# Optimization experiments

Hardware: AMD Instinct MI355X
Metric: run time of the kernel (lower is better)

The kernel has to match this reference:

```python
import jax, jax.numpy as jnp
import numpy as np

TOP_K = 5
MIN_DIST = 10
SALIENCY_THR = 0.1
BLUR_K = 5
BLUR_SIGMA = 1.0
BORDER = 12
Q = 0.9
CAND_MULT = 16  # candidate pool = TOP_K * CAND_MULT before min-dist suppression


def _hann(n):
    # torch.hann_window(n, periodic=False)
    return 0.5 * (1.0 - jnp.cos(2.0 * jnp.pi * jnp.arange(n, dtype=jnp.float32) / (n - 1)))


def _gauss_kernel2d():
    r = BLUR_K // 2
    x = jnp.arange(-r, r + 1, dtype=jnp.float32)
    g = jnp.exp(-(x ** 2) / (2.0 * BLUR_SIGMA ** 2))
    g = g / g.sum()
    k2 = g[:, None] * g[None, :]
    return k2[None, None]  # [1,1,k,k]


def _phase_saliency(img):
    """Phase-spectrum saliency: window -> FFT -> phase-only -> iFFT -> |.|^2 -> blur -> minmax norm -> border mask."""
    B, C, H, W = img.shape
    win = (_hann(H)[:, None] * _hann(W)[None, :])[None, None]  # [1,1,H,W]
    x = img * win
    f = jnp.fft.fft2(x)
    recon = jnp.fft.ifft2(jnp.exp(1j * jnp.angle(f)))
    sal = jnp.abs(recon) ** 2
    pad = BLUR_K // 2
    sal = jax.lax.conv_general_dilated(
        sal, _gauss_kernel2d(), (1, 1), [(pad, pad), (pad, pad)],
        dimension_numbers=("NCHW", "OIHW", "NCHW"))
    mn = sal.min(axis=(2, 3), keepdims=True)
    mx = sal.max(axis=(2, 3), keepdims=True)
    sal = (sal - mn) / (mx - mn + 1e-8)
    border = jnp.zeros((H, W), jnp.float32).at[BORDER:H - BORDER, BORDER:W - BORDER].set(1.0)
    return sal * border


def _dynamic_threshold(sal):
    # thr = value of the k-th largest pixel, k = (1-q)*N  (matches torch.topk(flat,k)[..., -1])
    B = sal.shape[0]
    flat = sal.reshape(B, -1)
    n = flat.shape[1]
    k = max(1, int((1.0 - Q) * n))
    vals = jax.lax.top_k(flat, k)[0]
    return vals[:, -1]  # [B]


def _select_points(sal2d, thr):
    """Greedy min-dist (NMS-style) selection of up to TOP_K peaks above thr. Returns (coords[K,2] xy, labels[K])."""
    H, W = sal2d.shape
    M = TOP_K * CAND_MULT
    scores = jnp.where(sal2d >= thr, sal2d, -jnp.inf).reshape(-1)
    vals, idx = jax.lax.top_k(scores, M)
    ys = (idx // W).astype(jnp.float32)
    xs = (idx % W).astype(jnp.float32)
    pts = jnp.stack([xs, ys], axis=-1)  # (x, y) ordering as in original
    valid = jnp.isfinite(vals)

    def body(i, state):
        keep, cnt = state
        d2 = jnp.sum((pts - pts[i]) ** 2, axis=-1)
        near_kept = jnp.any((d2 < float(MIN_DIST ** 2)) & keep)
        ok = valid[i] & (~near_kept) & (cnt < TOP_K)
        return keep.at[i].set(ok), cnt + ok.astype(jnp.int32)

    keep, _ = jax.lax.fori_loop(0, M, body, (jnp.zeros((M,), bool), jnp.int32(0)))
    order = jnp.argsort(jnp.where(keep, 0, 1).astype(jnp.int32))  # stable: kept (in score order) first
    sel = order[:TOP_K]
    kept = keep[sel]
    coords = jnp.where(kept[:, None], pts[sel], -1.0)
    labels = jnp.where(kept, 1, -1).astype(jnp.int32)
    return coords, labels


def setup_inputs() -> dict:
    key = jax.random.key(0)
    img = jax.random.uniform(key, (16, 1, 512, 512), dtype=jnp.float32)
    return {"img": img}


def reference(img):
    sal = _phase_saliency(img)                      # [B,1,H,W]
    thr = jnp.maximum(_dynamic_threshold(sal), SALIENCY_THR)  # dynamic_thr_mode='max'
    coords, labels = jax.vmap(_select_points)(sal[:, 0], thr)
    return coords, labels, sal
```

## Files before the change

### kernel.cpp

```cpp
#include <hip/hip_runtime.h>
#include <math.h>

#define BATCH 16
#define HW 262144
#define KSEL 26214
#define MCAND 80
#define TOPK 5
#define CAP 2048
#define ZEROWORDS 204816


#define GW0 0.05448868454964294f
#define GW1 0.24420134200323332f
#define GW2 0.40261994689424746f

#define FILL_TW512(nthr)                                       \
    for (int i_ = threadIdx.x; i_ < 256; i_ += (nthr)) {       \
        float rev_ = -(float)i_ * (1.0f / 512.0f);             \
        float s_ = __builtin_amdgcn_sinf(rev_);                \
        float c_ = __builtin_amdgcn_cosf(rev_);                \
        tws[i_] = s_;        twc[i_] = c_;                     \
        tws[i_ + 256] = -s_; twc[i_ + 256] = -c_;              \
    }

#define RP(a) ((a) + ((a) >> 4))
#define RSZ 544

#define R4_FWD(rr, ri, q, s4)                                                 \
    {                                                                          \
        const int log2n = 9 - 2 * (s4);                                        \
        const int log2m = log2n - 2;                                           \
        const int m = 1 << log2m;                                              \
        int r = (q) & (m - 1);                                                 \
        int j0 = (((q) >> log2m) << log2n) + r;                                \
        float a0x = rr[RP(j0)],       a0y = ri[RP(j0)];                        \
        float a1x = rr[RP(j0 + m)],   a1y = ri[RP(j0 + m)];                    \
        float a2x = rr[RP(j0 + 2*m)], a2y = ri[RP(j0 + 2*m)];                  \
        float a3x = rr[RP(j0 + 3*m)], a3y = ri[RP(j0 + 3*m)];                  \
        float s02x = a0x + a2x, s02y = a0y + a2y;                              \
        float d02x = a0x - a2x, d02y = a0y - a2y;                              \
        float s13x = a1x + a3x, s13y = a1y + a3y;                              \
        float d13x = a1x - a3x, d13y = a1y - a3y;                              \
        float y0x = s02x + s13x, y0y = s02y + s13y;                            \
        float y2x = s02x - s13x, y2y = s02y - s13y;                            \
        float y1x = d02x + d13y, y1y = d02y - d13x;                            \
        float y3x = d02x - d13y, y3y = d02y + d13x;                            \
        int e = r << (2 * (s4));                                               \
        float c1 = twc[e],   s1 = tws[e];                                      \
        float c2 = twc[2*e], s2 = tws[2*e];                                    \
        float c3 = twc[3*e], s3 = tws[3*e];                                    \
        rr[RP(j0)]       = y0x;             ri[RP(j0)]       = y0y;            \
        rr[RP(j0 + m)]   = y1x*c1 - y1y*s1; ri[RP(j0 + m)]   = y1x*s1 + y1y*c1;\
        rr[RP(j0 + 2*m)] = y2x*c2 - y2y*s2; ri[RP(j0 + 2*m)] = y2x*s2 + y2y*c2;\
        rr[RP(j0 + 3*m)] = y3x*c3 - y3y*s3; ri[RP(j0 + 3*m)] = y3x*s3 + y3y*c3;\
    }

#define R4_INV(rr, ri, q, s4)                                                 \
    {                                                                          \
        const int log2n = 9 - 2 * (s4);                                        \
        const int log2m = log2n - 2;                                           \
        const int m = 1 << log2m;                                              \
        int r = (q) & (m - 1);                                                 \
        int j0 = (((q) >> log2m) << log2n) + r;                                \
        float a0x = rr[RP(j0)],       a0y = ri[RP(j0)];                        \
        float a1x = rr[RP(j0 + m)],   a1y = ri[RP(j0 + m)];                    \
        float a2x = rr[RP(j0 + 2*m)], a2y = ri[RP(j0 + 2*m)];                  \
        float a3x = rr[RP(j0 + 3*m)], a3y = ri[RP(j0 + 3*m)];                  \
        int e = r << (2 * (s4));                                               \
        float c1 = twc[e],   s1 = tws[e];                                      \
        float c2 = twc[2*e], s2 = tws[2*e];                                    \
        float c3 = twc[3*e], s3 = tws[3*e];                                    \
        float t1x = a1x*c1 + a1y*s1,  t1y = a1y*c1 - a1x*s1;                   \
        float t2x = a2x*c2 + a2y*s2,  t2y = a2y*c2 - a2x*s2;                   \
        float t3x = a3x*c3 + a3y*s3,  t3y = a3y*c3 - a3x*s3;                   \
        float s02x = a0x + t2x, s02y = a0y + t2y;                              \
        float d02x = a0x - t2x, d02y = a0y - t2y;                              \
        float s13x = t1x + t3x, s13y = t1y + t3y;                              \
        float d13x = t1x - t3x, d13y = t1y - t3y;                              \
        rr[RP(j0)]       = s02x + s13x;  ri[RP(j0)]       = s02y + s13y;       \
        rr[RP(j0 + 2*m)] = s02x - s13x;  ri[RP(j0 + 2*m)] = s02y - s13y;       \
        rr[RP(j0 + m)]   = d02x - d13y;  ri[RP(j0 + m)]   = d02y + d13x;       \
        rr[RP(j0 + 3*m)] = d02x + d13y;  ri[RP(j0 + 3*m)] = d02y - d13x;       \
    }

__global__ void k_win_rowfft(const float* __restrict__ img, float2* __restrict__ A) {
    __shared__ float re[2 * RSZ], im[2 * RSZ];
    __shared__ float twc[512], tws[512];
    int t = threadIdx.x;
    FILL_TW512(256)
    int lr = t >> 7;
    int u  = t & 127;
    int row = blockIdx.x * 2 + lr;
    int h = row & 511;
    float wr = 0.5f * (1.0f - __builtin_amdgcn_cosf((float)h * (1.0f / 511.0f)));
    const float* p = img + (size_t)row * 512;
    float* rr = re + lr * RSZ;
    float* ri = im + lr * RSZ;
    {
        int i0 = u * 4;
        float4 v = *reinterpret_cast<const float4*>(p + i0);
        float w0 = 0.5f * (1.0f - __builtin_amdgcn_cosf((float)(i0 + 0) * (1.0f / 511.0f)));
        float w1 = 0.5f * (1.0f - __builtin_amdgcn_cosf((float)(i0 + 1) * (1.0f / 511.0f)));
        float w2 = 0.5f * (1.0f - __builtin_amdgcn_cosf((float)(i0 + 2) * (1.0f / 511.0f)));
        float w3 = 0.5f * (1.0f - __builtin_amdgcn_cosf((float)(i0 + 3) * (1.0f / 511.0f)));
        rr[RP(i0 + 0)] = v.x * wr * w0;  ri[RP(i0 + 0)] = 0.0f;
        rr[RP(i0 + 1)] = v.y * wr * w1;  ri[RP(i0 + 1)] = 0.0f;
        rr[RP(i0 + 2)] = v.z * wr * w2;  ri[RP(i0 + 2)] = 0.0f;
        rr[RP(i0 + 3)] = v.w * wr * w3;  ri[RP(i0 + 3)] = 0.0f;
    }
    __syncthreads();
    R4_FWD(rr, ri, u, 0)  __syncthreads();
    R4_FWD(rr, ri, u, 1)  __syncthreads();
    R4_FWD(rr, ri, u, 2)  __syncthreads();
    R4_FWD(rr, ri, u, 3)  __syncthreads();
    #pragma unroll
    for (int kk = 0; kk < 2; ++kk) {
        int j = (kk * 128 + u) << 1;
        float ax = rr[RP(j)], ay = ri[RP(j)], bx = rr[RP(j + 1)], by = ri[RP(j + 1)];
        rr[RP(j)]     = ax + bx;  ri[RP(j)]     = ay + by;
        rr[RP(j + 1)] = ax - bx;  ri[RP(j + 1)] = ay - by;
    }
    __syncthreads();
    float2* out = A + (size_t)row * 512;
    #pragma unroll
    for (int k2 = 0; k2 < 2; ++k2) {
        int i = u * 4 + k2 * 2;
        float4 v = make_float4(rr[RP(i)], ri[RP(i)], rr[RP(i + 1)], ri[RP(i + 1)]);
        *reinterpret_cast<float4*>(&out[i]) = v;
    }
}

#define CSTR 514
__global__ __launch_bounds__(512) void k_colfft(float2* __restrict__ X) {
    __shared__ float re[16 * CSTR];
    __shared__ float im[16 * CSTR];
    __shared__ float twc[512], tws[512];
    int b = blockIdx.x >> 5;
    int c0 = (blockIdx.x & 31) * 16;
    int t = threadIdx.x;
    FILL_TW512(512)
    float2* base = X + (size_t)b * HW + c0;
    #pragma unroll
    for (int ii = 0; ii < 8; ++ii) {
        int linear = ii * 512 + t;
        int cp = linear & 7;
        int e  = linear >> 3;
        const float4 v = *reinterpret_cast<const float4*>(&base[(size_t)e * 512 + cp * 2]);
        int a0 = (cp * 2) * CSTR + e;
        int a1 = a0 + CSTR;
        re[a0] = v.x; im[a0] = v.y;
        re[a1] = v.z; im[a1] = v.w;
    }
    __syncthreads();
    int c = t & 15, tt = t >> 4;
    float* cr = re + c * CSTR;
    float* ci = im + c * CSTR;

    for (int s4 = 0; s4 < 4; ++s4) {
        int log2n = 9 - 2 * s4;
        int log2m = log2n - 2;
        int m = 1 << log2m;
        #pragma unroll
        for (int kk = 0; kk < 4; ++kk) {
            int q = kk * 32 + tt;
            int r = q & (m - 1);
            int j0 = ((q >> log2m) << log2n) + r;
            float a0x = cr[j0],       a0y = ci[j0];
            float a1x = cr[j0 + m],   a1y = ci[j0 + m];
            float a2x = cr[j0 + 2*m], a2y = ci[j0 + 2*m];
            float a3x = cr[j0 + 3*m], a3y = ci[j0 + 3*m];
            float s02x = a0x + a2x, s02y = a0y + a2y;
            float d02x = a0x - a2x, d02y = a0y - a2y;
            float s13x = a1x + a3x, s13y = a1y + a3y;
            float d13x = a1x - a3x, d13y = a1y - a3y;
            float y0x = s02x + s13x, y0y = s02y + s13y;
            float y2x = s02x - s13x, y2y = s02y - s13y;
            float y1x = d02x + d13y, y1y = d02y - d13x;
            float y3x = d02x - d13y, y3y = d02y + d13x;
            int e = r << (2 * s4);
            float c1 = twc[e],   s1 = tws[e];
            float c2 = twc[2*e], s2 = tws[2*e];
            float c3 = twc[3*e], s3 = tws[3*e];
            cr[j0]       = y0x;                 ci[j0]       = y0y;
            cr[j0 + m]   = y1x*c1 - y1y*s1;     ci[j0 + m]   = y1x*s1 + y1y*c1;
            cr[j0 + 2*m] = y2x*c2 - y2y*s2;     ci[j0 + 2*m] = y2x*s2 + y2y*c2;
            cr[j0 + 3*m] = y3x*c3 - y3y*s3;     ci[j0 + 3*m] = y3x*s3 + y3y*c3;
        }
        __syncthreads();
    }
    #pragma unroll
    for (int kk = 0; kk < 8; ++kk) {
        int j = (kk * 32 + tt) << 1;
        float ax = cr[j], ay = ci[j], bx = cr[j+1], by = ci[j+1];
        cr[j]   = ax + bx; ci[j]   = ay + by;
        cr[j+1] = ax - bx; ci[j+1] = ay - by;
    }
    __syncthreads();
    #pragma unroll
    for (int ii = 0; ii < 16; ++ii) {
        int linear = ii * 512 + t;
        int cc = linear & 15, e = linear >> 4;
        int a = cc * CSTR + e;
        float x = re[a], y = im[a];
        float m2 = x * x + y * y;
        if (m2 > 0.0f) {
            float inv = rsqrtf(m2);
            re[a] = x * inv; im[a] = y * inv;
        } else {
            re[a] = 1.0f; im[a] = 0.0f;
        }
    }
    __syncthreads();
    #pragma unroll
    for (int kk = 0; kk < 8; ++kk) {
        int j = (kk * 32 + tt) << 1;
        float ax = cr[j], ay = ci[j], bx = cr[j+1], by = ci[j+1];
        cr[j]   = ax + bx; ci[j]   = ay + by;
        cr[j+1] = ax - bx; ci[j+1] = ay - by;
    }
    __syncthreads();
    for (int s4 = 3; s4 >= 0; --s4) {
        int log2n = 9 - 2 * s4;
        int log2m = log2n - 2;
        int m = 1 << log2m;
        #pragma unroll
        for (int kk = 0; kk < 4; ++kk) {
            int q = kk * 32 + tt;
            int r = q & (m - 1);
            int j0 = ((q >> log2m) << log2n) + r;
            float a0x = cr[j0],       a0y = ci[j0];
            float a1x = cr[j0 + m],   a1y = ci[j0 + m];
            float a2x = cr[j0 + 2*m], a2y = ci[j0 + 2*m];
            float a3x = cr[j0 + 3*m], a3y = ci[j0 + 3*m];
            int e = r << (2 * s4);
            float c1 = twc[e],   s1 = tws[e];
            float c2 = twc[2*e], s2 = tws[2*e];
            float c3 = twc[3*e], s3 = tws[3*e];
            float t1x = a1x*c1 + a1y*s1,  t1y = a1y*c1 - a1x*s1;
            float t2x = a2x*c2 + a2y*s2,  t2y = a2y*c2 - a2x*s2;
            float t3x = a3x*c3 + a3y*s3,  t3y = a3y*c3 - a3x*s3;
            float s02x = a0x + t2x, s02y = a0y + t2y;
            float d02x = a0x - t2x, d02y = a0y - t2y;
            float s13x = t1x + t3x, s13y = t1y + t3y;
            float d13x = t1x - t3x, d13y = t1y - t3y;
            cr[j0]       = s02x + s13x;   ci[j0]       = s02y + s13y;
            cr[j0 + 2*m] = s02x - s13x;   ci[j0 + 2*m] = s02y - s13y;
            cr[j0 + m]   = d02x - d13y;   ci[j0 + m]   = d02y + d13x;
            cr[j0 + 3*m] = d02x + d13y;   ci[j0 + 3*m] = d02y - d13x;
        }
        __syncthreads();
    }
    #pragma unroll
    for (int ii = 0; ii < 8; ++ii) {
        int linear = ii * 512 + t;
        int cp = linear & 7;
        int e  = linear >> 3;
        int a0 = (cp * 2) * CSTR + e;
        int a1 = a0 + CSTR;
        float4 v = make_float4(re[a0], im[a0], re[a1], im[a1]);
        *reinterpret_cast<float4*>(&base[(size_t)e * 512 + cp * 2]) = v;
    }
}

__global__ void k_mag_hblur(const float2* __restrict__ X, float* __restrict__ out) {
    __shared__ float re[2 * RSZ], im[2 * RSZ];
    __shared__ float twc[512], tws[512];
    int t = threadIdx.x;
    FILL_TW512(256)
    int lr = t >> 7;
    int u  = t & 127;
    int row = blockIdx.x * 2 + lr;
    const float2* p = X + (size_t)row * 512;
    float* rr = re + lr * RSZ;
    float* ri = im + lr * RSZ;
    #pragma unroll
    for (int k2 = 0; k2 < 2; ++k2) {
        int i = u * 4 + k2 * 2;
        float4 v = *reinterpret_cast<const float4*>(&p[i]);
        rr[RP(i)]     = v.x; ri[RP(i)]     = v.y;
        rr[RP(i + 1)] = v.z; ri[RP(i + 1)] = v.w;
    }
    __syncthreads();
    #pragma unroll
    for (int kk = 0; kk < 2; ++kk) {
        int j = (kk * 128 + u) << 1;
        float ax = rr[RP(j)], ay = ri[RP(j)], bx = rr[RP(j + 1)], by = ri[RP(j + 1)];
        rr[RP(j)]     = ax + bx;  ri[RP(j)]     = ay + by;
        rr[RP(j + 1)] = ax - bx;  ri[RP(j + 1)] = ay - by;
    }
    __syncthreads();
    R4_INV(rr, ri, u, 3)  __syncthreads();
    R4_INV(rr, ri, u, 2)  __syncthreads();
    R4_INV(rr, ri, u, 1)  __syncthreads();
    R4_INV(rr, ri, u, 0)  __syncthreads();
    const float s = 3.814697265625e-06f;
    #pragma unroll
    for (int k4 = 0; k4 < 4; ++k4) {
        int i = u * 4 + k4;
        float x = rr[RP(i)] * s, y = ri[RP(i)] * s;
        ri[RP(i)] = x * x + y * y;
    }
    __syncthreads();
    float* o = out + (size_t)row * 512;
    float4 res;
    #pragma unroll
    for (int k4 = 0; k4 < 4; ++k4) {
        int i = u * 4 + k4;
        float acc = GW2 * ri[RP(i)];
        if (i >= 1)   acc += GW1 * ri[RP(i - 1)];
        if (i >= 2)   acc += GW0 * ri[RP(i - 2)];
        if (i <= 510) acc += GW1 * ri[RP(i + 1)];
        if (i <= 509) acc += GW0 * ri[RP(i + 2)];
        ((float*)&res)[k4] = acc;
    }
    *reinterpret_cast<float4*>(o + u * 4) = res;
}

__global__ void k_vblur(const float* __restrict__ in, float* __restrict__ out,
                        float* __restrict__ pmn, float* __restrict__ pmx,
                        unsigned int* __restrict__ zr) {
    __shared__ float smn[256];
    __shared__ float smx[256];
    int t = threadIdx.x;
    int gi = blockIdx.x * 256 + t;
    if (gi < ZEROWORDS) zr[gi] = 0u;
    int i = gi * 4;
    int y = (i >> 9) & 511;
    const float4 c = *reinterpret_cast<const float4*>(in + i);
    float4 acc = make_float4(GW2 * c.x, GW2 * c.y, GW2 * c.z, GW2 * c.w);
    if (y >= 1) {
        const float4 v = *reinterpret_cast<const float4*>(in + i - 512);
        acc.x += GW1 * v.x; acc.y += GW1 * v.y; acc.z += GW1 * v.z; acc.w += GW1 * v.w;
    }
    if (y >= 2) {
        const float4 v = *reinterpret_cast<const float4*>(in + i - 1024);
        acc.x += GW0 * v.x; acc.y += GW0 * v.y; acc.z += GW0 * v.z; acc.w += GW0 * v.w;
    }
    if (y <= 510) {
        const float4 v = *reinterpret_cast<const float4*>(in + i + 512);
        acc.x += GW1 * v.x; acc.y += GW1 * v.y; acc.z += GW1 * v.z; acc.w += GW1 * v.w;
    }
    if (y <= 509) {
        const float4 v = *reinterpret_cast<const float4*>(in + i + 1024);
        acc.x += GW0 * v.x; acc.y += GW0 * v.y; acc.z += GW0 * v.z; acc.w += GW0 * v.w;
    }
    *reinterpret_cast<float4*>(out + i) = acc;
    float lmn = fminf(fminf(acc.x, acc.y), fminf(acc.z, acc.w));
    float lmx = fmaxf(fmaxf(acc.x, acc.y), fmaxf(acc.z, acc.w));
    smn[t] = lmn; smx[t] = lmx;
    __syncthreads();
    for (int s = 128; s > 0; s >>= 1) {
        if (t < s) { smn[t] = fminf(smn[t], smn[t + s]); smx[t] = fmaxf(smx[t], smx[t + s]); }
        __syncthreads();
    }
    if (t == 0) { pmn[blockIdx.x] = smn[0]; pmx[blockIdx.x] = smx[0]; }
}

__global__ void k_norm_hist(const float* __restrict__ in, const float* __restrict__ pmn,
                            const float* __restrict__ pmx, float* __restrict__ out,
                            unsigned int* __restrict__ g) {
    __shared__ unsigned int h[4096];
    __shared__ float smn[256], smx[256];
    int t = threadIdx.x;
    int b = blockIdx.x >> 5;
    int base = b * HW + (blockIdx.x & 31) * 8192;
    smn[t] = pmn[b * 256 + t];
    smx[t] = pmx[b * 256 + t];
    for (int i = t; i < 4096; i += 256) h[i] = 0u;
    __syncthreads();
    for (int s = 128; s > 0; s >>= 1) {
        if (t < s) { smn[t] = fminf(smn[t], smn[t + s]); smx[t] = fmaxf(smx[t], smx[t + s]); }
        __syncthreads();
    }
    float mn = smn[0], mx = smx[0];
    float inv = 1.0f / (mx - mn + 1e-8f);
    for (int j = 0; j < 32; ++j) {
        int idx = base + j * 256 + t;
        float v = (in[idx] - mn) * inv;
        int xx = idx & 511, yy = (idx >> 9) & 511;
        bool inside = (xx >= 12) && (xx < 500) && (yy >= 12) && (yy < 500);
        v = inside ? v : 0.0f;
        out[idx] = v;
        atomicAdd(&h[__float_as_uint(v) >> 20], 1u);
    }
    __syncthreads();
    unsigned int* gb = g + b * 4096;
    for (int i = t; i < 4096; i += 256)
        if (h[i]) atomicAdd(&gb[i], h[i]);
}

__device__ void radix_step(const unsigned int* __restrict__ h, int nbins, int krem,
                           int t, unsigned int* tsuf, int* sbin, int* skrem) {
    int bpt = nbins >> 8;
    unsigned int s = 0;
    for (int j = 0; j < bpt; ++j) s += h[t * bpt + j];
    tsuf[t] = s;
    __syncthreads();
    #pragma unroll
    for (int off = 1; off < 256; off <<= 1) {
        unsigned int v = (t + off < 256) ? tsuf[t + off] : 0u;
        __syncthreads();
        tsuf[t] += v;
        __syncthreads();
    }
    if ((int)tsuf[t] >= krem && (t == 255 || (int)tsuf[t + 1] < krem))
        *sbin = t;
    __syncthreads();
    int seg = *sbin;
    int krem2 = krem - (seg < 255 ? (int)tsuf[seg + 1] : 0);
    __syncthreads();
    if (t < bpt) {
        unsigned int L = 0;
        for (int j = t; j < bpt; ++j) L += h[seg * bpt + j];
        unsigned int hv = h[seg * bpt + t];
        if ((int)L >= krem2 && (int)(L - hv) < krem2) {
            *sbin  = seg * bpt + t;
            *skrem = krem2 - (int)(L - hv);
        }
    }
    __syncthreads();
}

__global__ void k_hist2(const float* __restrict__ sal, const unsigned int* __restrict__ g1,
                        unsigned int* __restrict__ gA, unsigned int* __restrict__ gB,
                        unsigned int* prefA1, int* kremA1, unsigned int* prefB1, int* kremB1) {
    __shared__ unsigned int hA[4096];
    __shared__ unsigned int hB[4096];
    __shared__ unsigned int tsuf[256];
    __shared__ int sbin, skrem;
    int t = threadIdx.x;
    int b = blockIdx.x >> 5;
    int start = (blockIdx.x & 31) * 8192;
    for (int i = t; i < 4096; i += 256) { hA[i] = 0u; hB[i] = 0u; }
    radix_step(g1 + b * 4096, 4096, KSEL, t, tsuf, &sbin, &skrem);
    unsigned int pA = (unsigned int)sbin; int krA = skrem;
    radix_step(g1 + b * 4096, 4096, MCAND, t, tsuf, &sbin, &skrem);
    unsigned int pB = (unsigned int)sbin; int krB = skrem;
    if (t == 0 && (blockIdx.x & 31) == 0) {
        prefA1[b] = pA; kremA1[b] = krA; prefB1[b] = pB; kremB1[b] = krB;
    }
    const float* p = sal + (size_t)b * HW;
    for (int j = 0; j < 32; ++j) {
        unsigned int u = __float_as_uint(p[start + j * 256 + t]);
        unsigned int hi = u >> 20, mid = (u >> 8) & 4095u;
        if (hi == pA) atomicAdd(&hA[mid], 1u);
        if (hi == pB) atomicAdd(&hB[mid], 1u);
    }
    __syncthreads();
    unsigned int* ga = gA + b * 4096;
    unsigned int* gb2 = gB + b * 4096;
    for (int i = t; i < 4096; i += 256) {
        if (hA[i]) atomicAdd(&ga[i], hA[i]);
        if (hB[i]) atomicAdd(&gb2[i], hB[i]);
    }
}

__global__ void k_hist3collect(const float* __restrict__ sal,
                               const unsigned int* __restrict__ gA2, const unsigned int* __restrict__ gB2,
                               const unsigned int* prefA1, const int* kremA1,
                               const unsigned int* prefB1, const int* kremB1,
                               unsigned int* __restrict__ gA3,
                               unsigned int* prefA24, int* kremA2,
                               float* __restrict__ candv, int* __restrict__ candi,
                               int* __restrict__ ccnt) {
    __shared__ unsigned int hA[256];
    __shared__ unsigned int tsuf[256];
    __shared__ int sbin, skrem;
    int t = threadIdx.x;
    int b = blockIdx.x >> 5;
    int start = (blockIdx.x & 31) * 8192;
    hA[t] = 0u;
    radix_step(gA2 + b * 4096, 4096, kremA1[b], t, tsuf, &sbin, &skrem);
    unsigned int pA = (prefA1[b] << 12) | (unsigned int)sbin;
    int krA2 = skrem;
    radix_step(gB2 + b * 4096, 4096, kremB1[b], t, tsuf, &sbin, &skrem);
    unsigned int cutB = ((prefB1[b] << 12) | (unsigned int)sbin) << 8;
    if (t == 0 && (blockIdx.x & 31) == 0) { prefA24[b] = pA; kremA2[b] = krA2; }
    const float* p = sal + (size_t)b * HW;
    for (int j = 0; j < 32; ++j) {
        int i = start + j * 256 + t;
        unsigned int u = __float_as_uint(p[i]);
        if ((u >> 8) == pA) atomicAdd(&hA[u & 255u], 1u);
        if (u >= cutB) {
            int pos = atomicAdd(&ccnt[b], 1);
            if (pos < CAP) { candv[b * CAP + pos] = p[i]; candi[b * CAP + pos] = i; }
        }
    }
    __syncthreads();
    if (hA[t]) atomicAdd(&gA3[b * 256 + t], hA[t]);
}

__global__ void k_final(const unsigned int* __restrict__ gA3,
                        const unsigned int* prefA24, const int* kremA2,
                        const float* __restrict__ candv, const int* __restrict__ candi,
                        const int* __restrict__ ccnt, float* __restrict__ out) {
    __shared__ float cval[CAP];
    __shared__ int   cidx[CAP];
    __shared__ int   si[MCAND];
    __shared__ float svv[MCAND];
    __shared__ float sx[MCAND];
    __shared__ float sy[MCAND];
    __shared__ unsigned long long nearLo[MCAND];
    __shared__ unsigned long long nearHi[MCAND];
    __shared__ unsigned int tsuf[256];
    __shared__ int sbin, skrem;
    int b = blockIdx.x, t = threadIdx.x;
    radix_step(gA3 + b * 256, 256, kremA2[b], t, tsuf, &sbin, &skrem);
    float thr = fmaxf(__uint_as_float((prefA24[b] << 8) | (unsigned int)sbin), 0.1f);
    int n = min(ccnt[b], CAP);
    for (int i = t; i < n; i += 256) { cval[i] = candv[b * CAP + i]; cidx[i] = candi[b * CAP + i]; }
    __syncthreads();
    int m = min(n, MCAND);
    for (int i = t; i < n; i += 256) {
        float vi = cval[i]; int ii = cidx[i];
        int rank = 0;
        for (int j = 0; j < n; j++) {
            float vj = cval[j];
            if (vj > vi || (vj == vi && cidx[j] < ii)) rank++;
        }
        if (rank < MCAND) { si[rank] = ii; svv[rank] = vi; }
    }
    __syncthreads();
    for (int i = t; i < m; i += 256) {
        sx[i] = (float)(si[i] & 511);
        sy[i] = (float)(si[i] >> 9);
    }
    __syncthreads();
    for (int i = t; i < m; i += 256) {
        unsigned long long lo = 0ull, hi = 0ull;
        float x = sx[i], y = sy[i];
        for (int j = 0; j < m; j++) {
            float dx = sx[j] - x, dy = sy[j] - y;
            if (dx * dx + dy * dy < 100.0f) {
                if (j < 64) lo |= (1ull << j);
                else        hi |= (1ull << (j - 64));
            }
        }
        nearLo[i] = lo; nearHi[i] = hi;
    }
    __syncthreads();
    if (t == 0) {
        unsigned long long kLo = 0ull, kHi = 0ull;
        int cnt = 0;
        for (int i = 0; i < m; i++) {
            bool near_kept = ((nearLo[i] & kLo) | (nearHi[i] & kHi)) != 0ull;
            if (svv[i] >= thr && !near_kept) {
                out[b * 10 + 2 * cnt]     = sx[i];
                out[b * 10 + 2 * cnt + 1] = sy[i];
                out[160 + b * 5 + cnt]    = 1.0f;
                if (i < 64) kLo |= (1ull << i); else kHi |= (1ull << (i - 64));
                cnt++;
                if (cnt == TOPK) break;
            }
        }
        for (int j = cnt; j < TOPK; j++) {
            out[b * 10 + 2 * j]     = -1.0f;
            out[b * 10 + 2 * j + 1] = -1.0f;
            out[160 + b * 5 + j]    = -1.0f;
        }
    }
}

extern "C" void kernel_launch(void* const* d_in, const int* in_sizes, int n_in,
                              void* d_out, int out_size, void* d_ws, size_t ws_size,
                              hipStream_t stream) {
    const float* img = (const float*)d_in[0];
    float* out = (float*)d_out;
    char* ws = (char*)d_ws;

    float2* A    = (float2*)ws;
    float*  hb   = (float*)(ws + 33554432UL);
    float*  salb = (float*)(ws + 50331648UL);

    unsigned int* hist1  = (unsigned int*)(ws + 0UL);
    unsigned int* hist2a = (unsigned int*)(ws + 262144UL);
    unsigned int* hist2b = (unsigned int*)(ws + 524288UL);
    unsigned int* hist3a = (unsigned int*)(ws + 786432UL);
    int*          ccnt   = (int*)(ws + 819200UL);
    float*        candv  = (float*)(ws + 851968UL);
    int*          candi  = (int*)(ws + 983040UL);

    float* pmn = (float*)(ws + 20971520UL);
    float* pmx = (float*)(ws + 21037056UL);

    char* stats = ws + 67108864UL;
    unsigned int* prefA1  = (unsigned int*)(stats + 0);
    int*          kremA1  = (int*)(stats + 64);
    unsigned int* prefB1  = (unsigned int*)(stats + 128);
    int*          kremB1  = (int*)(stats + 192);
    unsigned int* prefA24 = (unsigned int*)(stats + 256);
    int*          kremA2  = (int*)(stats + 320);

    float* salout = out + 240;

    k_win_rowfft<<<dim3(4096), dim3(256), 0, stream>>>(img, A);
    k_colfft<<<dim3(512), dim3(512), 0, stream>>>(A);
    k_mag_hblur<<<dim3(4096), dim3(256), 0, stream>>>(A, hb);
    k_vblur<<<dim3(4096), dim3(256), 0, stream>>>(hb, salb, pmn, pmx,
                                                  (unsigned int*)ws);
    k_norm_hist<<<dim3(512), dim3(256), 0, stream>>>(salb, pmn, pmx, salout, hist1);
    k_hist2<<<dim3(512), dim3(256), 0, stream>>>(salout, hist1, hist2a, hist2b,
                                                 prefA1, kremA1, prefB1, kremB1);
    k_hist3collect<<<dim3(512), dim3(256), 0, stream>>>(salout, hist2a, hist2b,
                                                        prefA1, kremA1, prefB1, kremB1,
                                                        hist3a, prefA24, kremA2,
                                                        candv, candi, ccnt);
    k_final<<<dim3(BATCH), dim3(256), 0, stream>>>(hist3a, prefA24, kremA2,
                                                   candv, candi, ccnt, out);
}
```

Before: 154.5 us.

## Fuse radix-4 column FFT stage pairs into register-resident radix-16 passes

Replaces the four shared-memory radix-4 stages of the column FFT, and their inverse, with two passes that each load 16 complex points per thread into registers, apply two radix-4 stages, and write back. This halves the shared-memory round trips and the __syncthreads barriers in the forward and inverse column transforms. The cost is higher register pressure from the 32-float register arrays, which could lower occupancy.

```diff
diff --git a/kernel.cpp b/kernel.cpp
--- a/kernel.cpp
+++ b/kernel.cpp
@@ -83,6 +83,33 @@
         rr[RP(j0 + 3*m)] = d02x + d13y;  ri[RP(j0 + 3*m)] = d02y - d13x;       \
     }
 
+#define R4F_REG(x0,y0,x1,y1,x2,y2,x3,y3, e)                                   \
+    { float s02x=(x0)+(x2), s02y=(y0)+(y2), d02x=(x0)-(x2), d02y=(y0)-(y2);    \
+      float s13x=(x1)+(x3), s13y=(y1)+(y3), d13x=(x1)-(x3), d13y=(y1)-(y3);    \
+      float z0x=s02x+s13x, z0y=s02y+s13y;                                      \
+      float z2x=s02x-s13x, z2y=s02y-s13y;                                      \
+      float z1x=d02x+d13y, z1y=d02y-d13x;                                      \
+      float z3x=d02x-d13y, z3y=d02y+d13x;                                      \
+      float c1=twc[(e)], s1=tws[(e)], c2=twc[2*(e)], s2=tws[2*(e)];            \
+      float c3=twc[3*(e)], s3=tws[3*(e)];                                      \
+      x0=z0x; y0=z0y;                                                          \
+      x1=z1x*c1-z1y*s1; y1=z1x*s1+z1y*c1;                                      \
+      x2=z2x*c2-z2y*s2; y2=z2x*s2+z2y*c2;                                      \
+      x3=z3x*c3-z3y*s3; y3=z3x*s3+z3y*c3; }
+
+#define R4I_REG(x0,y0,x1,y1,x2,y2,x3,y3, e)                                   \
+    { float c1=twc[(e)], s1=tws[(e)], c2=twc[2*(e)], s2=tws[2*(e)];            \
+      float c3=twc[3*(e)], s3=tws[3*(e)];                                      \
+      float t1x=(x1)*c1+(y1)*s1, t1y=(y1)*c1-(x1)*s1;                          \
+      float t2x=(x2)*c2+(y2)*s2, t2y=(y2)*c2-(x2)*s2;                          \
+      float t3x=(x3)*c3+(y3)*s3, t3y=(y3)*c3-(x3)*s3;                          \
+      float s02x=(x0)+t2x, s02y=(y0)+t2y, d02x=(x0)-t2x, d02y=(y0)-t2y;        \
+      float s13x=t1x+t3x, s13y=t1y+t3y, d13x=t1x-t3x, d13y=t1y-t3y;            \
+      x0=s02x+s13x; y0=s02y+s13y;                                              \
+      x2=s02x-s13x; y2=s02y-s13y;                                              \
+      x1=d02x-d13y; y1=d02y+d13x;                                              \
+      x3=d02x+d13y; y3=d02y-d13x; }
+
 __global__ void k_win_rowfft(const float* __restrict__ img, float2* __restrict__ A) {
     __shared__ float re[2 * RSZ], im[2 * RSZ];
     __shared__ float twc[512], tws[512];
@@ -155,39 +182,69 @@
     int c = t & 15, tt = t >> 4;
     float* cr = re + c * CSTR;
     float* ci = im + c * CSTR;
-
-    for (int s4 = 0; s4 < 4; ++s4) {
-        int log2n = 9 - 2 * s4;
-        int log2m = log2n - 2;
-        int m = 1 << log2m;
-        #pragma unroll
-        for (int kk = 0; kk < 4; ++kk) {
-            int q = kk * 32 + tt;
-            int r = q & (m - 1);
-            int j0 = ((q >> log2m) << log2n) + r;
-            float a0x = cr[j0],       a0y = ci[j0];
-            float a1x = cr[j0 + m],   a1y = ci[j0 + m];
-            float a2x = cr[j0 + 2*m], a2y = ci[j0 + 2*m];
-            float a3x = cr[j0 + 3*m], a3y = ci[j0 + 3*m];
-            float s02x = a0x + a2x, s02y = a0y + a2y;
-            float d02x = a0x - a2x, d02y = a0y - a2y;
-            float s13x = a1x + a3x, s13y = a1y + a3y;
-            float d13x = a1x - a3x, d13y = a1y - a3y;
-            float y0x = s02x + s13x, y0y = s02y + s13y;
-            float y2x = s02x - s13x, y2y = s02y - s13y;
-            float y1x = d02x + d13y, y1y = d02y - d13x;
-            float y3x = d02x - d13y, y3y = d02y + d13x;
-            int e = r << (2 * s4);
-            float c1 = twc[e],   s1 = tws[e];
-            float c2 = twc[2*e], s2 = tws[2*e];
-            float c3 = twc[3*e], s3 = tws[3*e];
-            cr[j0]       = y0x;                 ci[j0]       = y0y;
-            cr[j0 + m]   = y1x*c1 - y1y*s1;     ci[j0 + m]   = y1x*s1 + y1y*c1;
-            cr[j0 + 2*m] = y2x*c2 - y2y*s2;     ci[j0 + 2*m] = y2x*s2 + y2y*c2;
-            cr[j0 + 3*m] = y3x*c3 - y3y*s3;     ci[j0 + 3*m] = y3x*s3 + y3y*c3;
-        }
-        __syncthreads();
-    }
+    float rx[4][4], ry[4][4];
+
+    #pragma unroll
+    for (int a = 0; a < 4; ++a)
+        #pragma unroll
+        for (int bq = 0; bq < 4; ++bq) {
+            int j = tt + a * 128 + bq * 32;
+            rx[a][bq] = cr[j]; ry[a][bq] = ci[j];
+        }
+    #pragma unroll
+    for (int bq = 0; bq < 4; ++bq) {
+        int e = tt + bq * 32;
+        R4F_REG(rx[0][bq], ry[0][bq], rx[1][bq], ry[1][bq],
+                rx[2][bq], ry[2][bq], rx[3][bq], ry[3][bq], e)
+    }
+    {
+        int e = tt << 2;
+        #pragma unroll
+        for (int a = 0; a < 4; ++a)
+            R4F_REG(rx[a][0], ry[a][0], rx[a][1], ry[a][1],
+                    rx[a][2], ry[a][2], rx[a][3], ry[a][3], e)
+    }
+    #pragma unroll
+    for (int a = 0; a < 4; ++a)
+        #pragma unroll
+        for (int bq = 0; bq < 4; ++bq) {
+            int j = tt + a * 128 + bq * 32;
+            cr[j] = rx[a][bq]; ci[j] = ry[a][bq];
+        }
+    __syncthreads();
+
+    {
+        int blk = tt >> 1, r = tt & 1;
+        int jb = blk * 32 + r;
+        #pragma unroll
+        for (int a = 0; a < 4; ++a)
+            #pragma unroll
+            for (int bq = 0; bq < 4; ++bq) {
+                int j = jb + a * 8 + bq * 2;
+                rx[a][bq] = cr[j]; ry[a][bq] = ci[j];
+            }
+        #pragma unroll
+        for (int bq = 0; bq < 4; ++bq) {
+            int e = (r + 2 * bq) << 4;
+            R4F_REG(rx[0][bq], ry[0][bq], rx[1][bq], ry[1][bq],
+                    rx[2][bq], ry[2][bq], rx[3][bq], ry[3][bq], e)
+        }
+        {
+            int e = r << 6;
+            #pragma unroll
+            for (int a = 0; a < 4; ++a)
+                R4F_REG(rx[a][0], ry[a][0], rx[a][1], ry[a][1],
+                        rx[a][2], ry[a][2], rx[a][3], ry[a][3], e)
+        }
+        #pragma unroll
+        for (int a = 0; a < 4; ++a)
+            #pragma unroll
+            for (int bq = 0; bq < 4; ++bq) {
+                int j = jb + a * 8 + bq * 2;
+                cr[j] = rx[a][bq]; ci[j] = ry[a][bq];
+            }
+    }
+    __syncthreads();
     #pragma unroll
     for (int kk = 0; kk < 8; ++kk) {
         int j = (kk * 32 + tt) << 1;
@@ -219,37 +276,66 @@
         cr[j+1] = ax - bx; ci[j+1] = ay - by;
     }
     __syncthreads();
-    for (int s4 = 3; s4 >= 0; --s4) {
-        int log2n = 9 - 2 * s4;
-        int log2m = log2n - 2;
-        int m = 1 << log2m;
-        #pragma unroll
-        for (int kk = 0; kk < 4; ++kk) {
-            int q = kk * 32 + tt;
-            int r = q & (m - 1);
-            int j0 = ((q >> log2m) << log2n) + r;
-            float a0x = cr[j0],       a0y = ci[j0];
-            float a1x = cr[j0 + m],   a1y = ci[j0 + m];
-            float a2x = cr[j0 + 2*m], a2y = ci[j0 + 2*m];
-            float a3x = cr[j0 + 3*m], a3y = ci[j0 + 3*m];
-            int e = r << (2 * s4);
-            float c1 = twc[e],   s1 = tws[e];
-            float c2 = twc[2*e], s2 = tws[2*e];
-            float c3 = twc[3*e], s3 = tws[3*e];
-            float t1x = a1x*c1 + a1y*s1,  t1y = a1y*c1 - a1x*s1;
-            float t2x = a2x*c2 + a2y*s2,  t2y = a2y*c2 - a2x*s2;
-            float t3x = a3x*c3 + a3y*s3,  t3y = a3y*c3 - a3x*s3;
-            float s02x = a0x + t2x, s02y = a0y + t2y;
-            float d02x = a0x - t2x, d02y = a0y - t2y;
-            float s13x = t1x + t3x, s13y = t1y + t3y;
-            float d13x = t1x - t3x, d13y = t1y - t3y;
-            cr[j0]       = s02x + s13x;   ci[j0]       = s02y + s13y;
-            cr[j0 + 2*m] = s02x - s13x;   ci[j0 + 2*m] = s02y - s13y;
-            cr[j0 + m]   = d02x - d13y;   ci[j0 + m]   = d02y + d13x;
-            cr[j0 + 3*m] = d02x + d13y;   ci[j0 + 3*m] = d02y - d13x;
-        }
-        __syncthreads();
-    }
+    {
+        int blk = tt >> 1, r = tt & 1;
+        int jb = blk * 32 + r;
+        #pragma unroll
+        for (int a = 0; a < 4; ++a)
+            #pragma unroll
+            for (int bq = 0; bq < 4; ++bq) {
+                int j = jb + a * 8 + bq * 2;
+                rx[a][bq] = cr[j]; ry[a][bq] = ci[j];
+            }
+        {
+            int e = r << 6;
+            #pragma unroll
+            for (int a = 0; a < 4; ++a)
+                R4I_REG(rx[a][0], ry[a][0], rx[a][1], ry[a][1],
+                        rx[a][2], ry[a][2], rx[a][3], ry[a][3], e)
+        }
+        #pragma unroll
+        for (int bq = 0; bq < 4; ++bq) {
+            int e = (r + 2 * bq) << 4;
+            R4I_REG(rx[0][bq], ry[0][bq], rx[1][bq], ry[1][bq],
+                    rx[2][bq], ry[2][bq], rx[3][bq], ry[3][bq], e)
+        }
+        #pragma unroll
+        for (int a = 0; a < 4; ++a)
+            #pragma unroll
+            for (int bq = 0; bq < 4; ++bq) {
+                int j = jb + a * 8 + bq * 2;
+                cr[j] = rx[a][bq]; ci[j] = ry[a][bq];
+            }
+    }
+    __syncthreads();
+    #pragma unroll
+    for (int a = 0; a < 4; ++a)
+        #pragma unroll
+        for (int bq = 0; bq < 4; ++bq) {
+            int j = tt + a * 128 + bq * 32;
+            rx[a][bq] = cr[j]; ry[a][bq] = ci[j];
+        }
+    {
+        int e = tt << 2;
+        #pragma unroll
+        for (int a = 0; a < 4; ++a)
+            R4I_REG(rx[a][0], ry[a][0], rx[a][1], ry[a][1],
+                    rx[a][2], ry[a][2], rx[a][3], ry[a][3], e)
+    }
+    #pragma unroll
+    for (int bq = 0; bq < 4; ++bq) {
+        int e = tt + bq * 32;
+        R4I_REG(rx[0][bq], ry[0][bq], rx[1][bq], ry[1][bq],
+                rx[2][bq], ry[2][bq], rx[3][bq], ry[3][bq], e)
+    }
+    #pragma unroll
+    for (int a = 0; a < 4; ++a)
+        #pragma unroll
+        for (int bq = 0; bq < 4; ++bq) {
+            int j = tt + a * 128 + bq * 32;
+            cr[j] = rx[a][bq]; ci[j] = ry[a][bq];
+        }
+    __syncthreads();
     #pragma unroll
     for (int ii = 0; ii < 8; ++ii) {
         int linear = ii * 512 + t;
```

Result: no change. 152.4 us (-1.4%).
